# Kernel optimization log

Measured on AMD Instinct MI355X. Metric: run time of the kernel, lower is better.

## Reference

```python
import jax, jax.numpy as jnp
import numpy as np

BN_EPS = 1e-5


def setup_inputs() -> dict:
    key = jax.random.key(0)
    ks = jax.random.split(key, 6)
    B, C, K, N = 4, 64, 16, 16384  # batch, feat channels, neighbors, points
    W_OUT = 16  # weightnet output channels (fixed by Linear(16*mlp[-1], ...))
    xyz = jax.random.normal(ks[0], (B, N, 3), dtype=jnp.float32)
    points = jax.random.normal(ks[1], (B, C, K, N), dtype=jnp.float32)
    coordinate = jax.random.normal(ks[2], (B, 3, K, N), dtype=jnp.float32)
    w1 = jax.random.normal(ks[3], (W_OUT, 3), dtype=jnp.float32) * 0.5
    b1 = jnp.zeros((W_OUT,), dtype=jnp.float32)
    lin_w = jax.random.normal(ks[4], (C, W_OUT * C), dtype=jnp.float32) * (1.0 / np.sqrt(W_OUT * C))
    lin_b = jnp.zeros((C,), dtype=jnp.float32)
    gamma = jnp.ones((C,), dtype=jnp.float32)
    beta = jnp.zeros((C,), dtype=jnp.float32)
    return {"xyz": xyz, "points": points, "coordinate": coordinate,
            "w1": w1, "b1": b1, "lin_w": lin_w, "lin_b": lin_b,
            "gamma": gamma, "beta": beta}


def reference(xyz, points, coordinate, w1, b1, lin_w, lin_b, gamma, beta):
    B, C, K, N = points.shape
    # weightnet: 1x1 conv (3 -> 16) + ReLU over coordinate [B,3,K,N] -> [B,16,K,N]
    weights = jax.nn.relu(jnp.einsum('oc,bckn->bokn', w1, coordinate) + b1[None, :, None, None])
    # per-point aggregation: [B,N,C,K] @ [B,N,K,16] -> [B,N,C,16]
    new_points = jnp.einsum('bckn,bokn->bnco', points, weights)
    new_points = new_points.reshape(B, N, C * 16)  # [B, N, 16*C]
    # linear projection 16*C -> C
    new_points = jnp.einsum('bnk,ok->bno', new_points, lin_w) + lin_b  # [B, N, C]
    # BatchNorm1d over channel dim (training-mode batch stats), layout [B, C, N]
    new_points = new_points.transpose(0, 2, 1)  # [B, C, N]
    mean = jnp.mean(new_points, axis=(0, 2), keepdims=True)
    var = jnp.var(new_points, axis=(0, 2), keepdims=True)
    new_points = (new_points - mean) * jax.lax.rsqrt(var + BN_EPS)
    new_points = new_points * gamma[None, :, None] + beta[None, :, None]
    new_points = jax.nn.relu(new_points)  # [B, C, N]
    return (xyz, new_points)
```

## Files before the change

kernel.cpp:

```cpp
#include <hip/hip_runtime.h>

#define BB 4
#define CC 64
#define KK 16
#define NN 16384
#define NTB 256

typedef __attribute__((ext_vector_type(8))) short short8;
typedef __attribute__((ext_vector_type(4))) float floatx4;
typedef __attribute__((ext_vector_type(2))) _Float16 half2v;

__device__ __forceinline__ unsigned short f2bf_rtne(float x) {
    unsigned u = __builtin_bit_cast(unsigned, x);
    u += 0x7FFFu + ((u >> 16) & 1u);
    return (unsigned short)(u >> 16);
}

__device__ __forceinline__ unsigned pack_bf16x2(float lo, float hi) {
    unsigned a = __builtin_bit_cast(unsigned, lo) + 0x8000u;
    unsigned b = __builtin_bit_cast(unsigned, hi) + 0x8000u;
    return __builtin_amdgcn_perm(b, a, 0x07060302u);
}

__device__ __forceinline__ half2v cvt2h(float a, float b) {
    return __builtin_bit_cast(half2v, __builtin_amdgcn_cvt_pkrtz(a, b));
}
__device__ __forceinline__ unsigned pk2u(float a, float b) {
    return __builtin_bit_cast(unsigned, __builtin_amdgcn_cvt_pkrtz(a, b));
}

#if __has_builtin(__builtin_amdgcn_fdot2)
#define DOT2(a, b, c) __builtin_amdgcn_fdot2((a), (b), (c), false)
#else
__device__ __forceinline__ float dot2_fb(half2v a, half2v b, float c) {
    return fmaf((float)a[0], (float)b[0], fmaf((float)a[1], (float)b[1], c));
}
#define DOT2(a, b, c) dot2_fb((a), (b), (c))
#endif

__global__ __launch_bounds__(256)
void prep_bfrag(const float* __restrict__ lin_w, unsigned short* __restrict__ bfrag,
                float* __restrict__ part)
{
    const int tid  = blockIdx.x * 256 + threadIdx.x;
    if (tid < 512) part[tid] = 0.0f;

    const int lane = tid & 63;
    const int g    = tid >> 6;
    const int ci   = g >> 4;
    const int kk   = (g >> 2) & 3;
    const int nt   = g & 3;
    const int r    = lane & 15;
    const int sq   = lane >> 4;

    const float* src = lin_w + (size_t)(nt * 16 + r) * 1024 + ci * 128 + kk * 32 + sq * 8;
    unsigned short v[8];
    #pragma unroll
    for (int j = 0; j < 8; ++j) v[j] = f2bf_rtne(src[j]);
    *(uint4*)(bfrag + ((size_t)g * 64 + lane) * 8) = *(const uint4*)v;
}

__global__ __launch_bounds__(512, 2)
void fused_main(const float* __restrict__ points,
                const float* __restrict__ coordinate,
                const float* __restrict__ w1,
                const float* __restrict__ b1,
                const unsigned short* __restrict__ bfrag,
                float* __restrict__ y_out,
                float* __restrict__ part)
{
    __shared__ unsigned int s_p[2][2][8][256];
    __shared__ uint4 s_a[4][2][1024];

    const int t    = threadIdx.x;
    const int lane = t & 63;
    const int wv   = __builtin_amdgcn_readfirstlane(t >> 6);
    const int P    = wv >> 1;
    const int h    = wv & 1;
    const int r    = lane & 15;
    const int sq   = lane >> 4;

    const int bid = blockIdx.x;
    const int b   = bid >> 6;
    const int n0b = (bid & 63) * NTB;
    const int n0p = n0b + P * 64;

    half2v wh[8][8];
    {
        const float* coordB = coordinate + (size_t)b * 3 * KK * NN + n0p + lane;
        float c0[KK], c1[KK], c2[KK];
        #pragma unroll
        for (int k = 0; k < KK; ++k) {
            c0[k] = coordB[(0 * KK + k) * NN];
            c1[k] = coordB[(1 * KK + k) * NN];
            c2[k] = coordB[(2 * KK + k) * NN];
        }
        #pragma unroll
        for (int j = 0; j < 8; ++j) {
            const int o = 8 * h + j;
            const float w1x = w1[o * 3 + 0];
            const float w1y = w1[o * 3 + 1];
            const float w1z = w1[o * 3 + 2];
            const float bo  = b1[o];
            #pragma unroll
            for (int kp = 0; kp < 8; ++kp) {
                float v0 = fmaf(w1x, c0[2 * kp],     fmaf(w1y, c1[2 * kp],     fmaf(w1z, c2[2 * kp],     bo)));
                float v1 = fmaf(w1x, c0[2 * kp + 1], fmaf(w1y, c1[2 * kp + 1], fmaf(w1z, c2[2 * kp + 1], bo)));
                wh[j][kp] = cvt2h(fmaxf(v0, 0.0f), fmaxf(v1, 0.0f));
            }
        }
    }

    floatx4 acc[2][4];
    #pragma unroll
    for (int m = 0; m < 2; ++m)
        #pragma unroll
        for (int nt = 0; nt < 4; ++nt) acc[m][nt] = (floatx4){0.f, 0.f, 0.f, 0.f};

    const float* pS = points + (size_t)b * CC * KK * NN + n0b + 4 * lane;

    float4 stF[2][2][2];

#define ISSUE(SLOT, G) {                                                        \
        const int cA = 2 * (G);                                                 \
        stF[SLOT][0][0] = *(const float4*)(pS + (size_t)(cA * 16 + 2 * wv) * NN);       \
        stF[SLOT][0][1] = *(const float4*)(pS + (size_t)(cA * 16 + 2 * wv + 1) * NN);   \
        stF[SLOT][1][0] = *(const float4*)(pS + (size_t)((cA + 1) * 16 + 2 * wv) * NN); \
        stF[SLOT][1][1] = *(const float4*)(pS + (size_t)((cA + 1) * 16 + 2 * wv + 1) * NN); }

#define WRITE(SLOT, BUF) {                                                      \
        _Pragma("unroll")                                                       \
        for (int ch = 0; ch < 2; ++ch) {                                        \
            const float4 A = stF[SLOT][ch][0], Bv = stF[SLOT][ch][1];           \
            uint4 W;                                                            \
            W.x = pk2u(A.x, Bv.x);  W.y = pk2u(A.y, Bv.y);                      \
            W.z = pk2u(A.z, Bv.z);  W.w = pk2u(A.w, Bv.w);                      \
            *(uint4*)&s_p[BUF][ch][wv][4 * lane] = W;                           \
        } }

#define CONSUME(GEXPR, BUF, GG) {                                               \
        const int g_ = (GEXPR);                                                 \
        _Pragma("unroll")                                                       \
        for (int chh = 0; chh < 2; ++chh) {                                     \
            const int cl = (2 * (GG) + chh) & 7;    \
            half2v ph[8];                                                       \
            _Pragma("unroll")                                                   \
            for (int kp = 0; kp < 8; ++kp)                                      \
                ph[kp] = __builtin_bit_cast(half2v, s_p[BUF][chh][kp][P * 64 + lane]); \
            float a8[8];                                                        \
            _Pragma("unroll")                                                   \
            for (int j = 0; j < 8; ++j) {                                       \
                float a = 0.f;                                                  \
                _Pragma("unroll")                                               \
                for (int kp = 0; kp < 8; ++kp) a = DOT2(ph[kp], wh[j][kp], a);  \
                a8[j] = a;                                                      \
            }                                                                   \
            uint4 pk;                                                           \
            pk.x = pack_bf16x2(a8[0], a8[1]);                                   \
            pk.y = pack_bf16x2(a8[2], a8[3]);                                   \
            pk.z = pack_bf16x2(a8[4], a8[5]);                                   \
            pk.w = pack_bf16x2(a8[6], a8[7]);                                   \
            s_a[P][((2 * g_ + chh) >> 3) & 1]                                   \
               [(lane >> 4) * 256 + (cl >> 1) * 64 + (lane & 15) * 4            \
                + (cl & 1) * 2 + h] = pk;                                       \
        } }

    ISSUE(0, 0)
    ISSUE(1, 1)
    WRITE(0, 0)
    asm volatile("s_waitcnt lgkmcnt(0)\n\ts_barrier" ::: "memory");

    for (int ci = 0; ci < 8; ++ci) {
        #pragma unroll
        for (int gg = 0; gg < 4; ++gg) {
            const int g = ci * 4 + gg;
            if (g + 2 < 32) ISSUE(gg & 1, g + 2)
            CONSUME(g, gg & 1, gg)
            if (g + 1 < 32) WRITE((gg + 1) & 1, (gg + 1) & 1)

            if (gg == 3) {
                uint4 bf_c[4];
                #pragma unroll
                for (int nt = 0; nt < 4; ++nt)
                    bf_c[nt] = *(const uint4*)(bfrag + ((((size_t)ci * 4 + 0) * 4 + nt) * 64 + lane) * 8);

                asm volatile("s_waitcnt lgkmcnt(0)\n\ts_barrier" ::: "memory");

                const uint4* saR = &s_a[P][ci & 1][0];
                #pragma unroll
                for (int kk = 0; kk < 4; ++kk) {
                    uint4 bf_n[4];
                    if (kk < 3) {
                        #pragma unroll
                        for (int nt = 0; nt < 4; ++nt)
                            bf_n[nt] = *(const uint4*)(bfrag + ((((size_t)ci * 4 + kk + 1) * 4 + nt) * 64 + lane) * 8);
                    }
                    short8 af[2];
                    #pragma unroll
                    for (int m = 0; m < 2; ++m)
                        af[m] = __builtin_bit_cast(short8, saR[(2 * h + m) * 256 + kk * 64 + r * 4 + sq]);
                    #pragma unroll
                    for (int m = 0; m < 2; ++m)
                        #pragma unroll
                        for (int nt = 0; nt < 4; ++nt)
                            acc[m][nt] = __builtin_amdgcn_mfma_f32_16x16x32_bf16(
                                af[m], __builtin_bit_cast(short8, bf_c[nt]), acc[m][nt], 0, 0, 0);
                    #pragma unroll
                    for (int nt = 0; nt < 4; ++nt) bf_c[nt] = bf_n[nt];
                }
            } else {
                asm volatile("s_waitcnt lgkmcnt(0)\n\ts_barrier" ::: "memory");
            }
        }
    }
#undef ISSUE
#undef WRITE
#undef CONSUME

    float* yB  = y_out + (size_t)b * CC * NN + n0p;
    float* sb  = (float*)&s_p[0][0][0][0];
    float* sb2 = sb + 1024;
    #pragma unroll
    for (int m = 0; m < 2; ++m)
        #pragma unroll
        for (int nt = 0; nt < 4; ++nt) {
            const int oc = nt * 16 + r;
            const floatx4 v = acc[m][nt];
            *(float4*)(yB + (size_t)oc * NN + (2 * h + m) * 16 + sq * 4) =
                make_float4(v[0], v[1], v[2], v[3]);

            float s  = v[0] + v[1] + v[2] + v[3];
            float ss = v[0] * v[0] + v[1] * v[1] + v[2] * v[2] + v[3] * v[3];
            s  += __shfl_xor(s, 16);  s  += __shfl_xor(s, 32);
            ss += __shfl_xor(ss, 16); ss += __shfl_xor(ss, 32);
            if (lane < 16) {
                sb [(wv * 2 + m) * 64 + oc] = s;
                sb2[(wv * 2 + m) * 64 + oc] = ss;
            }
        }
    __syncthreads();
    if (t < 64) {
        float S = 0.f, SS = 0.f;
        #pragma unroll
        for (int q = 0; q < 16; ++q) {
            S  += sb [q * 64 + t];
            SS += sb2[q * 64 + t];
        }
        atomicAdd(&part[b * 64 + t], S);
        atomicAdd(&part[256 + b * 64 + t], SS);
    }
}

__global__ void bn_stats(const float* __restrict__ part,
                         const float* __restrict__ gamma,
                         const float* __restrict__ beta,
                         float* __restrict__ ab)
{
    const int ch = threadIdx.x;
    float S = 0.f, SS = 0.f;
    #pragma unroll
    for (int b = 0; b < BB; ++b) {
        S  += part[b * 64 + ch];
        SS += part[256 + b * 64 + ch];
    }
    const float inv  = 1.0f / (float)(BB * NN);
    const float mean = S * inv;
    const float var  = SS * inv - mean * mean;
    const float a    = gamma[ch] * rsqrtf(var + 1e-5f);
    ab[ch]      = a;
    ab[CC + ch] = beta[ch] - mean * a;
}

__global__ __launch_bounds__(256)
void bn_apply(float* __restrict__ y, const float* __restrict__ ab)
{
    const size_t i = (size_t)blockIdx.x * 256 + threadIdx.x;
    float4* p = (float4*)y;
    float4 v = p[i];
    const int ch = (int)((i * 4) >> 14) & 63;
    const float a = ab[ch], bb = ab[CC + ch];
    v.x = fmaxf(fmaf(a, v.x, bb), 0.0f);
    v.y = fmaxf(fmaf(a, v.y, bb), 0.0f);
    v.z = fmaxf(fmaf(a, v.z, bb), 0.0f);
    v.w = fmaxf(fmaf(a, v.w, bb), 0.0f);
    p[i] = v;
}

extern "C" void kernel_launch(void* const* d_in, const int* in_sizes, int n_in,
                              void* d_out, int out_size, void* d_ws, size_t ws_size,
                              hipStream_t stream)
{
    const float* xyz        = (const float*)d_in[0];
    const float* points     = (const float*)d_in[1];
    const float* coordinate = (const float*)d_in[2];
    const float* w1         = (const float*)d_in[3];
    const float* b1         = (const float*)d_in[4];
    const float* lin_w      = (const float*)d_in[5];
    const float* gamma      = (const float*)d_in[7];
    const float* beta       = (const float*)d_in[8];

    float* out = (float*)d_out;

    unsigned short* bfrag = (unsigned short*)d_ws;
    float* part = (float*)d_ws + 32768;
    float* ab   = part + 512;

    const size_t xyz_elems = (size_t)BB * NN * 3;
    (void)hipMemcpyAsync(out, xyz, xyz_elems * sizeof(float),
                         hipMemcpyDeviceToDevice, stream);

    float* y_out = out + xyz_elems;

    prep_bfrag<<<32, 256, 0, stream>>>(lin_w, bfrag, part);
    fused_main<<<BB * (NN / NTB), 512, 0, stream>>>(
        points, coordinate, w1, b1, bfrag, y_out, part);
    bn_stats<<<1, 64, 0, stream>>>(part, gamma, beta, ab);
    bn_apply<<<(BB * CC * NN) / 4 / 256, 256, 0, stream>>>(y_out, ab);
}
```

Measured before the change: 395.7 us.

## Deepen global prefetch to four slots and fold BN stats into apply kernel

The register staging for points loads grows from two to four slots, so global loads are issued four groups ahead of consumption instead of two, hiding more memory latency in the main fused kernel. Separately, the single-block bn_stats kernel is removed and each bn_apply block recomputes the per-channel scale and shift into shared memory, saving one kernel launch and its serialization. The deeper prefetch costs extra VGPRs (16 more float4 registers), which may reduce occupancy or cause spills; the redundant per-block stats computation adds a small amount of work per block.

```diff
diff --git a/kernel.cpp b/kernel.cpp
--- a/kernel.cpp
+++ b/kernel.cpp
@@ -119,7 +119,7 @@
 
     const float* pS = points + (size_t)b * CC * KK * NN + n0b + 4 * lane;
 
-    float4 stF[2][2][2];
+    float4 stF[4][2][2];
 
 #define ISSUE(SLOT, G) {                                                        \
         const int cA = 2 * (G);                                                 \
@@ -167,6 +167,8 @@
 
     ISSUE(0, 0)
     ISSUE(1, 1)
+    ISSUE(2, 2)
+    ISSUE(3, 3)
     WRITE(0, 0)
     asm volatile("s_waitcnt lgkmcnt(0)\n\ts_barrier" ::: "memory");
 
@@ -174,9 +176,9 @@
         #pragma unroll
         for (int gg = 0; gg < 4; ++gg) {
             const int g = ci * 4 + gg;
-            if (g + 2 < 32) ISSUE(gg & 1, g + 2)
-            CONSUME(g, gg & 1, gg)
-            if (g + 1 < 32) WRITE((gg + 1) & 1, (gg + 1) & 1)
+            if (g + 4 < 32) ISSUE(g & 3, g + 4)
+            CONSUME(g, g & 1, gg)
+            if (g + 1 < 32) WRITE((g + 1) & 3, (g + 1) & 1)
 
             if (gg == 3) {
                 uint4 bf_c[4];
@@ -251,34 +253,33 @@
     }
 }
 
-__global__ void bn_stats(const float* __restrict__ part,
-                         const float* __restrict__ gamma,
-                         const float* __restrict__ beta,
-                         float* __restrict__ ab)
+__global__ __launch_bounds__(256)
+void bn_apply(float* __restrict__ y, const float* __restrict__ part,
+              const float* __restrict__ gamma, const float* __restrict__ beta)
 {
-    const int ch = threadIdx.x;
-    float S = 0.f, SS = 0.f;
-    #pragma unroll
-    for (int b = 0; b < BB; ++b) {
-        S  += part[b * 64 + ch];
-        SS += part[256 + b * 64 + ch];
+    __shared__ float sab[2 * CC];
+    if (threadIdx.x < CC) {
+        const int ch = threadIdx.x;
+        float S = 0.f, SS = 0.f;
+        #pragma unroll
+        for (int bb = 0; bb < BB; ++bb) {
+            S  += part[bb * 64 + ch];
+            SS += part[256 + bb * 64 + ch];
+        }
+        const float inv  = 1.0f / (float)(BB * NN);
+        const float mean = S * inv;
+        const float var  = SS * inv - mean * mean;
+        const float a    = gamma[ch] * rsqrtf(var + 1e-5f);
+        sab[ch]      = a;
+        sab[CC + ch] = beta[ch] - mean * a;
     }
-    const float inv  = 1.0f / (float)(BB * NN);
-    const float mean = S * inv;
-    const float var  = SS * inv - mean * mean;
-    const float a    = gamma[ch] * rsqrtf(var + 1e-5f);
-    ab[ch]      = a;
-    ab[CC + ch] = beta[ch] - mean * a;
-}
-
-__global__ __launch_bounds__(256)
-void bn_apply(float* __restrict__ y, const float* __restrict__ ab)
-{
+    __syncthreads();
+
     const size_t i = (size_t)blockIdx.x * 256 + threadIdx.x;
     float4* p = (float4*)y;
     float4 v = p[i];
     const int ch = (int)((i * 4) >> 14) & 63;
-    const float a = ab[ch], bb = ab[CC + ch];
+    const float a = sab[ch], bb = sab[CC + ch];
     v.x = fmaxf(fmaf(a, v.x, bb), 0.0f);
     v.y = fmaxf(fmaf(a, v.y, bb), 0.0f);
     v.z = fmaxf(fmaf(a, v.z, bb), 0.0f);
@@ -303,7 +304,6 @@
 
     unsigned short* bfrag = (unsigned short*)d_ws;
     float* part = (float*)d_ws + 32768;
-    float* ab   = part + 512;
 
     const size_t xyz_elems = (size_t)BB * NN * 3;
     (void)hipMemcpyAsync(out, xyz, xyz_elems * sizeof(float),
@@ -314,6 +314,5 @@
     prep_bfrag<<<32, 256, 0, stream>>>(lin_w, bfrag, part);
     fused_main<<<BB * (NN / NTB), 512, 0, stream>>>(
         points, coordinate, w1, b1, bfrag, y_out, part);
-    bn_stats<<<1, 64, 0, stream>>>(part, gamma, beta, ab);
-    bn_apply<<<(BB * CC * NN) / 4 / 256, 256, 0, stream>>>(y_out, ab);
-}
+    bn_apply<<<(BB * CC * NN) / 4 / 256, 256, 0, stream>>>(y_out, part, gamma, beta);
+}
```

Result: no change. 397.4 us (+0.4%).
